# Performance work log

Measured on AMD Instinct MI355X. Metric: run time of the kernel, lower is better.

Reference implementation:

```python
import jax, jax.numpy as jnp
import numpy as np

EPS = 1e-12

def _layernorm(x, gamma, beta):
    m = jnp.mean(x, axis=-1, keepdims=True)
    v = jnp.mean((x - m) ** 2, axis=-1, keepdims=True)
    return (x - m) * jax.lax.rsqrt(v + EPS) * gamma + beta

def _gcn(x, node_emb, time_emb, W_pool, b_pool, gamma, beta):
    # x: [B, N, C]; node_emb: [N, D]; time_emb: [D]
    e = _layernorm(node_emb + time_emb[None, :], gamma, beta)          # [N, D] (dropout off: eval mode)
    A = jax.nn.softmax(e @ e.T, axis=1)                                 # [N, N] dynamic adjacency
    weights = jnp.einsum('nd,dkio->nkio', e, W_pool)                    # [N, 2, C, O] node-adaptive weights
    bias = e @ b_pool                                                   # [N, O]
    # supports = [I, A]; I support is identity -> x itself
    x_g = jnp.stack([x, jnp.einsum('nm,bmc->bnc', A, x)], axis=2)       # [B, N, 2, C]
    return jnp.einsum('bnki,nkio->bno', x_g, weights) + bias            # [B, N, O]

def setup_inputs() -> dict:
    key = jax.random.key(0)
    ks = jax.random.split(key, 16)
    B, N, Din, H, D = 64, 2048, 2, 64, 16
    C = Din + H
    inp = {
        'x': jax.random.normal(ks[0], (B, N, Din), jnp.float32),
        'state': jax.random.normal(ks[1], (B, N, H), jnp.float32),
        'node_embeddings': jax.random.normal(ks[2], (N, D), jnp.float32),
        'time_embeddings': jax.random.normal(ks[3], (D,), jnp.float32),
    }
    for i, g in enumerate(['z', 'r', 'u']):
        inp[f'W_{g}'] = jax.random.normal(ks[4 + 2 * i], (D, 2, C, H), jnp.float32) * 0.02
        inp[f'b_{g}'] = jax.random.normal(ks[5 + 2 * i], (D, H), jnp.float32) * 0.02
        inp[f'gamma_{g}'] = jnp.ones((D,), jnp.float32)
        inp[f'beta_{g}'] = jnp.zeros((D,), jnp.float32)
    return inp

def reference(x, state, node_embeddings, time_embeddings,
              W_z, b_z, gamma_z, beta_z,
              W_r, b_r, gamma_r, beta_r,
              W_u, b_u, gamma_u, beta_u):
    xs = jnp.concatenate([x, state], axis=-1)                           # [B, N, Din+H]
    z = jax.nn.sigmoid(_gcn(xs, node_embeddings, time_embeddings, W_z, b_z, gamma_z, beta_z))
    r = jax.nn.sigmoid(_gcn(xs, node_embeddings, time_embeddings, W_r, b_r, gamma_r, beta_r))
    cand = jnp.concatenate([x, z * state], axis=-1)
    hc = jnp.tanh(_gcn(cand, node_embeddings, time_embeddings, W_u, b_u, gamma_u, beta_u))
    return r * state + (1.0 - r) * hc
```

## Files before the change

### kernel.cpp

```cpp
#include <hip/hip_runtime.h>
#include <hip/hip_bf16.h>
#include <math.h>


typedef __attribute__((ext_vector_type(4))) float f4;
typedef __attribute__((ext_vector_type(8))) short s8;

#define B_   64
#define N_   2048
#define DIN  2
#define H_   64
#define D_   16
#define C_   66
#define KI   132
#define KIP  160
#define CB   4224

#define GLD16(gp, lp) __builtin_amdgcn_global_load_lds((const __attribute__((address_space(1))) void*)(gp), (__attribute__((address_space(3))) void*)(lp), 16, 0, 0)

static __device__ __forceinline__ ushort f2bf(float v) {
  __hip_bfloat16 h = __float2bfloat16(v);
  return *(ushort*)&h;
}
static __device__ __forceinline__ float bf2f(ushort u) {
  __hip_bfloat16 h = *(__hip_bfloat16*)&u;
  return __bfloat162float(h);
}
static __device__ __forceinline__ uint packbf(float a, float b) {
  return ((uint)f2bf(b) << 16) | f2bf(a);
}

__global__ void k_e(const float* __restrict__ node, const float* __restrict__ timee,
                    const float* __restrict__ g0, const float* __restrict__ b0,
                    const float* __restrict__ g1, const float* __restrict__ b1,
                    const float* __restrict__ g2, const float* __restrict__ b2,
                    float* __restrict__ e) {
  int n = blockIdx.x * blockDim.x + threadIdx.x;
  if (n >= N_) return;
  float v[D_]; float m = 0.f;
  #pragma unroll
  for (int d = 0; d < D_; ++d) { v[d] = node[n * D_ + d] + timee[d]; m += v[d]; }
  m *= (1.0f / D_);
  float var = 0.f;
  #pragma unroll
  for (int d = 0; d < D_; ++d) { float t = v[d] - m; var += t * t; }
  var *= (1.0f / D_);
  float r = rsqrtf(var + 1e-12f);
  #pragma unroll
  for (int d = 0; d < D_; ++d) {
    float y = (v[d] - m) * r;
    e[0 * N_ * D_ + n * D_ + d] = y * g0[d] + b0[d];
    e[1 * N_ * D_ + n * D_ + d] = y * g1[d] + b1[d];
    e[2 * N_ * D_ + n * D_ + d] = y * g2[d] + b2[d];
  }
}

__global__ __launch_bounds__(256)
void k_S(const float* __restrict__ e, float* __restrict__ S) {
  __shared__ __align__(16) ushort At[128 * 32];
  __shared__ __align__(16) ushort Bt[128 * 32];
  const int t = threadIdx.x;
  const int c0 = blockIdx.x * 128, r0 = blockIdx.y * 128;
  const float* eg = e + (size_t)blockIdx.z * (N_ * D_);
  float* Sg = S + (size_t)blockIdx.z * ((size_t)N_ * N_);
  const int row = t >> 1, half = t & 1;
  {
    const float* p = eg + (size_t)(r0 + row) * D_ + half * 8;
    float4 a = *(const float4*)p, b = *(const float4*)(p + 4);
    ushort pk[8] = {f2bf(a.x), f2bf(a.y), f2bf(a.z), f2bf(a.w), f2bf(b.x), f2bf(b.y), f2bf(b.z), f2bf(b.w)};
    *(uint4*)&At[row * 32 + half * 8] = *(uint4*)pk;
    uint4 z = {0, 0, 0, 0};
    *(uint4*)&At[row * 32 + 16 + half * 8] = z;
    const float* q2 = eg + (size_t)(c0 + row) * D_ + half * 8;
    float4 c = *(const float4*)q2, d = *(const float4*)(q2 + 4);
    ushort pk2[8] = {f2bf(c.x), f2bf(c.y), f2bf(c.z), f2bf(c.w), f2bf(d.x), f2bf(d.y), f2bf(d.z), f2bf(d.w)};
    *(uint4*)&Bt[row * 32 + half * 8] = *(uint4*)pk2;
    *(uint4*)&Bt[row * 32 + 16 + half * 8] = z;
  }
  __syncthreads();
  const int l15 = t & 15, q = (t >> 4) & 3, w = t >> 6;
  const int wr = (w >> 1) * 64, wc = (w & 1) * 64;
  s8 af[4], bf[4];
  #pragma unroll
  for (int mi = 0; mi < 4; ++mi) af[mi] = *(const s8*)&At[(wr + mi * 16 + l15) * 32 + q * 8];
  #pragma unroll
  for (int ni = 0; ni < 4; ++ni) bf[ni] = *(const s8*)&Bt[(wc + ni * 16 + l15) * 32 + q * 8];
  f4 acc[4][4];
  #pragma unroll
  for (int i = 0; i < 4; ++i)
    #pragma unroll
    for (int j = 0; j < 4; ++j) acc[i][j] = (f4)0.0f;
  #pragma unroll
  for (int mi = 0; mi < 4; ++mi)
    #pragma unroll
    for (int ni = 0; ni < 4; ++ni)
      acc[mi][ni] = __builtin_amdgcn_mfma_f32_16x16x32_bf16(af[mi], bf[ni], acc[mi][ni], 0, 0, 0);
  #pragma unroll
  for (int mi = 0; mi < 4; ++mi) {
    int rr = r0 + wr + mi * 16 + q * 4;
    #pragma unroll
    for (int ni = 0; ni < 4; ++ni) {
      int cc = c0 + wc + ni * 16 + l15;
      #pragma unroll
      for (int rg = 0; rg < 4; ++rg)
        Sg[(size_t)(rr + rg) * N_ + cc] = acc[mi][ni][rg];
    }
  }
}

__global__ __launch_bounds__(256)
void k_rowsm(const float* __restrict__ S, __hip_bfloat16* __restrict__ A) {
  __shared__ float red[256];
  const int r = blockIdx.x, t = threadIdx.x;
  const float* Sr = S + (size_t)blockIdx.z * ((size_t)N_ * N_) + (size_t)r * N_;
  float4 v0 = ((const float4*)Sr)[t];
  float4 v1 = ((const float4*)Sr)[t + 256];
  float mx = fmaxf(fmaxf(fmaxf(v0.x, v0.y), fmaxf(v0.z, v0.w)),
                   fmaxf(fmaxf(v1.x, v1.y), fmaxf(v1.z, v1.w)));
  red[t] = mx; __syncthreads();
  for (int st = 128; st > 0; st >>= 1) { if (t < st) red[t] = fmaxf(red[t], red[t + st]); __syncthreads(); }
  const float gmax = red[0]; __syncthreads();
  float e0 = __expf(v0.x - gmax), e1 = __expf(v0.y - gmax), e2 = __expf(v0.z - gmax), e3 = __expf(v0.w - gmax);
  float e4 = __expf(v1.x - gmax), e5 = __expf(v1.y - gmax), e6 = __expf(v1.z - gmax), e7 = __expf(v1.w - gmax);
  red[t] = e0 + e1 + e2 + e3 + e4 + e5 + e6 + e7; __syncthreads();
  for (int st = 128; st > 0; st >>= 1) { if (t < st) red[t] += red[t + st]; __syncthreads(); }
  const float inv = 1.0f / red[0];
  ushort* Ar = (ushort*)A + (size_t)blockIdx.z * ((size_t)N_ * N_) + (size_t)r * N_;
  ushort p0[4] = {f2bf(e0 * inv), f2bf(e1 * inv), f2bf(e2 * inv), f2bf(e3 * inv)};
  ushort p1[4] = {f2bf(e4 * inv), f2bf(e5 * inv), f2bf(e6 * inv), f2bf(e7 * inv)};
  *(uint2*)&Ar[t * 4] = *(uint2*)p0;
  *(uint2*)&Ar[1024 + t * 4] = *(uint2*)p1;
}

template <int MODE>
__global__ __launch_bounds__(256)
void k_buildX(const float* __restrict__ x, const float* __restrict__ state,
              const __hip_bfloat16* __restrict__ zbuf, __hip_bfloat16* __restrict__ XT) {
  constexpr int LDM = 72;
  __shared__ __align__(16) ushort T[C_ * LDM];
  const int t = threadIdx.x;
  const int m0 = blockIdx.x * 64, b = blockIdx.y;
  const int m = t >> 2, hq = t & 3;
  {
    const float* sp = state + ((size_t)b * N_ + m0 + m) * H_ + hq * 16;
    float sv[16];
    #pragma unroll
    for (int i = 0; i < 16; i += 4) {
      float4 v = *(const float4*)(sp + i);
      sv[i] = v.x; sv[i + 1] = v.y; sv[i + 2] = v.z; sv[i + 3] = v.w;
    }
    if (MODE) {
      const ushort* zp = (const ushort*)zbuf + ((size_t)b * N_ + m0 + m) * H_ + hq * 16;
      uint4 z0 = *(const uint4*)&zp[0], z1 = *(const uint4*)&zp[8];
      uint zw[8] = {z0.x, z0.y, z0.z, z0.w, z1.x, z1.y, z1.z, z1.w};
      #pragma unroll
      for (int i = 0; i < 8; ++i) {
        sv[2 * i]     *= bf2f((ushort)(zw[i] & 0xffffu));
        sv[2 * i + 1] *= bf2f((ushort)(zw[i] >> 16));
      }
    }
    #pragma unroll
    for (int i = 0; i < 16; ++i) T[(DIN + hq * 16 + i) * LDM + m] = f2bf(sv[i]);
    if (t < 64) {
      const float2 xv = *(const float2*)&x[((size_t)b * N_ + m0 + t) * DIN];
      T[0 * LDM + t] = f2bf(xv.x);
      T[1 * LDM + t] = f2bf(xv.y);
    }
  }
  __syncthreads();
  {
    int r = t >> 2, ch = t & 3;
    ushort* dst = (ushort*)XT + (size_t)(b * C_ + r) * N_ + m0 + ch * 16;
    *(uint4*)&dst[0] = *(uint4*)&T[r * LDM + ch * 16];
    *(uint4*)&dst[8] = *(uint4*)&T[r * LDM + ch * 16 + 8];
    if (t < 8) {
      r = 64 + (t >> 2);
      ushort* dst2 = (ushort*)XT + (size_t)(b * C_ + r) * N_ + m0 + ch * 16;
      *(uint4*)&dst2[0] = *(uint4*)&T[r * LDM + ch * 16];
      *(uint4*)&dst2[8] = *(uint4*)&T[r * LDM + ch * 16 + 8];
    }
  }
}

__global__ __launch_bounds__(256)
void k_gemm(const __hip_bfloat16* __restrict__ Abase, size_t astride,
            const __hip_bfloat16* __restrict__ XT,
            __hip_bfloat16* __restrict__ Ybase, size_t ystride) {
  __shared__ __align__(16) ushort At[128 * 32];
  __shared__ __align__(16) ushort Xt[128 * 32];
  const int t = threadIdx.x;
  const int j0 = blockIdx.x * 128, r0 = blockIdx.y * 128;
  const ushort* Ag = (const ushort*)Abase + (size_t)blockIdx.z * astride;
  ushort* Y = (ushort*)Ybase + (size_t)blockIdx.z * ystride;
  const int lane = t & 63, w = t >> 6;
  const int rowa = w * 32 + (lane >> 2), kc = (lane & 3) * 8;
  const ushort* gA = Ag + (size_t)(r0 + rowa) * N_ + kc;
  const ushort* gX = (const ushort*)XT + (size_t)(j0 + rowa) * N_ + kc;
  ushort* lA0 = &At[(w * 32) * 32];
  ushort* lA1 = &At[(w * 32 + 16) * 32];
  ushort* lX0 = &Xt[(w * 32) * 32];
  ushort* lX1 = &Xt[(w * 32 + 16) * 32];
  const int l15 = t & 15, q = (t >> 4) & 3;
  const int wr = (w >> 1) * 64, wc = (w & 1) * 64;
  f4 acc[4][4];
  #pragma unroll
  for (int i = 0; i < 4; ++i)
    #pragma unroll
    for (int jj = 0; jj < 4; ++jj) acc[i][jj] = (f4)0.0f;
  for (int k0 = 0; k0 < N_; k0 += 32) {
    __syncthreads();
    GLD16(gA + k0, lA0);
    GLD16(gA + 16 * N_ + k0, lA1);
    GLD16(gX + k0, lX0);
    GLD16(gX + 16 * N_ + k0, lX1);
    __syncthreads();
    s8 af[4], bf[4];
    #pragma unroll
    for (int mi = 0; mi < 4; ++mi) af[mi] = *(const s8*)&At[(wr + mi * 16 + l15) * 32 + q * 8];
    #pragma unroll
    for (int ni = 0; ni < 4; ++ni) bf[ni] = *(const s8*)&Xt[(wc + ni * 16 + l15) * 32 + q * 8];
    #pragma unroll
    for (int mi = 0; mi < 4; ++mi)
      #pragma unroll
      for (int ni = 0; ni < 4; ++ni)
        acc[mi][ni] = __builtin_amdgcn_mfma_f32_16x16x32_bf16(af[mi], bf[ni], acc[mi][ni], 0, 0, 0);
  }
  #pragma unroll
  for (int mi = 0; mi < 4; ++mi) {
    int rr = r0 + wr + mi * 16 + q * 4;
    #pragma unroll
    for (int ni = 0; ni < 4; ++ni) {
      int cc = j0 + wc + ni * 16 + l15;
      #pragma unroll
      for (int rg = 0; rg < 4; ++rg)
        Y[(size_t)(rr + rg) * CB + cc] = f2bf(acc[mi][ni][rg]);
    }
  }
}

__global__ __launch_bounds__(256)
void k_wmat(const float* __restrict__ eg, const float* __restrict__ Wp, ushort* __restrict__ Wm) {
  constexpr int TRS = 36;
  __shared__ float Wl[16 * 8 * 64];
  __shared__ ushort Tr[8 * 64 * TRS];
  const int t = threadIdx.x;
  const int n0 = blockIdx.x * 8;
  const int y = blockIdx.y;
  const int o = t & 63, w = t >> 6;
  const int ng = w & 1, krh = (w >> 1) * 4;
  float er[4][16];
  #pragma unroll
  for (int j = 0; j < 4; ++j) {
    const float* ep = eg + (size_t)(n0 + ng * 4 + j) * D_;
    #pragma unroll
    for (int d = 0; d < D_; d += 4) {
      float4 v = *(const float4*)(ep + d);
      er[j][d] = v.x; er[j][d + 1] = v.y; er[j][d + 2] = v.z; er[j][d + 3] = v.w;
    }
  }
  const int ngroups = (y == 3) ? 2 : 1;
  for (int g = 0; g < ngroups; ++g) {
    const int kic0 = y * 4 + g * 4;
    for (int kk = 0; kk < 4; ++kk) {
      const int kic = kic0 + kk;
      __syncthreads();
      #pragma unroll
      for (int it = 0; it < 8; ++it) {
        int f = it * 256 + t;
        int d = f >> 7, rem = f & 127, kr = rem >> 4, o4 = rem & 15;
        int ki = kic * 8 + kr;
        float4 v;
        if (ki < KI) v = *(const float4*)&Wp[((size_t)d * KI + ki) * 64 + o4 * 4];
        else { v.x = 0.f; v.y = 0.f; v.z = 0.f; v.w = 0.f; }
        *(float4*)&Wl[f * 4] = v;
      }
      __syncthreads();
      float a[4][4];
      #pragma unroll
      for (int j = 0; j < 4; ++j)
        #pragma unroll
        for (int k = 0; k < 4; ++k) a[j][k] = 0.f;
      for (int d = 0; d < D_; ++d) {
        float w4[4];
        #pragma unroll
        for (int k = 0; k < 4; ++k) w4[k] = Wl[(d * 8 + krh + k) * 64 + o];
        #pragma unroll
        for (int j = 0; j < 4; ++j)
          #pragma unroll
          for (int k = 0; k < 4; ++k) a[j][k] = fmaf(er[j][d], w4[k], a[j][k]);
      }
      #pragma unroll
      for (int j = 0; j < 4; ++j) {
        ushort* tr = &Tr[((ng * 4 + j) * 64 + o) * TRS + kk * 8 + krh];
        *(uint*)&tr[0] = packbf(a[j][0], a[j][1]);
        *(uint*)&tr[2] = packbf(a[j][2], a[j][3]);
      }
    }
    __syncthreads();
    const int k0 = kic0 * 8;
    #pragma unroll
    for (int p = 0; p < 8; ++p) {
      int u = p * 256 + t;
      int nl = u >> 8, oo = (u >> 2) & 63, q = u & 3;
      const ushort* tr = &Tr[(nl * 64 + oo) * TRS + q * 8];
      uint2 lo = *(const uint2*)&tr[0];
      uint2 hi = *(const uint2*)&tr[4];
      uint4 vv; vv.x = lo.x; vv.y = lo.y; vv.z = hi.x; vv.w = hi.y;
      *(uint4*)&Wm[((size_t)(n0 + nl) * 64 + oo) * KIP + k0 + q * 8] = vv;
    }
  }
}

template <int MODE>
__global__ __launch_bounds__(256)
void k_einsum(const float* __restrict__ e, const ushort* __restrict__ Wm, const float* __restrict__ bp,
              const __hip_bfloat16* __restrict__ Y,
              const float* __restrict__ x, const float* __restrict__ state,
              const __hip_bfloat16* __restrict__ zbuf, const __hip_bfloat16* __restrict__ rbuf,
              void* __restrict__ outp) {
  constexpr int LDK = 168;
  constexpr int LDR = 72;
  __shared__ __align__(16) ushort xg[64 * LDK];
  __shared__ __align__(16) ushort res[64 * LDR];
  __shared__ float el[D_];
  __shared__ float bl[64];
  const int n = blockIdx.x, t = threadIdx.x;
  if (t < D_) el[t] = e[n * D_ + t];
  __syncthreads();
  if (t < 64) {
    float s = 0.f;
    #pragma unroll
    for (int d = 0; d < D_; ++d) s += el[d] * bp[d * 64 + t];
    bl[t] = s;
  }
  {
    const int b = t >> 2, j = t & 3;
    const size_t bn = (size_t)b * N_ + n;
    float sv[16];
    const float* sp = state + bn * 64 + j * 16;
    #pragma unroll
    for (int i = 0; i < 16; i += 4) {
      float4 v = *(const float4*)(sp + i);
      sv[i] = v.x; sv[i + 1] = v.y; sv[i + 2] = v.z; sv[i + 3] = v.w;
    }
    if (MODE) {
      const ushort* zp = (const ushort*)zbuf + bn * 64 + j * 16;
      uint4 z0 = *(const uint4*)&zp[0], z1 = *(const uint4*)&zp[8];
      uint zw[8] = {z0.x, z0.y, z0.z, z0.w, z1.x, z1.y, z1.z, z1.w};
      #pragma unroll
      for (int i = 0; i < 8; ++i) {
        sv[2 * i]     *= bf2f((ushort)(zw[i] & 0xffffu));
        sv[2 * i + 1] *= bf2f((ushort)(zw[i] >> 16));
      }
    }
    ushort* xr = &xg[b * LDK + 2 + j * 16];
    #pragma unroll
    for (int i = 0; i < 16; i += 2) {
      uint pk = packbf(sv[i], sv[i + 1]);
      *(uint*)&xr[i] = pk;
    }
    const ushort* yp = (const ushort*)Y + (size_t)n * CB + b * C_ + j * 16;
    uint* xy = (uint*)&xg[b * LDK + 66 + j * 16];
    #pragma unroll
    for (int i = 0; i < 8; ++i) xy[i] = *(const uint*)&yp[2 * i];
    if (j == 0) *(uint*)&xg[b * LDK + 130] = *(const uint*)&yp[64];
    if (t < 64) {
      const float* xp = x + ((size_t)t * N_ + n) * DIN;
      uint pk = packbf(xp[0], xp[1]);
      *(uint*)&xg[t * LDK] = pk;
    }
    ushort* pg = &xg[b * LDK + 132 + j * 7];
    #pragma unroll
    for (int i = 0; i < 7; ++i) pg[i] = 0;
  }
  __syncthreads();
  const int l15 = t & 15, q = (t >> 4) & 3, w = t >> 6;
  const int wm = (w >> 1) * 32, wn = (w & 1) * 32;
  const ushort* Wn = Wm + (size_t)n * (64 * KIP);
  f4 acc[2][2];
  acc[0][0] = acc[0][1] = acc[1][0] = acc[1][1] = (f4)0.0f;
  #pragma unroll
  for (int kk = 0; kk < KIP; kk += 32) {
    s8 af[2], bfr[2];
    #pragma unroll
    for (int mi = 0; mi < 2; ++mi) af[mi] = *(const s8*)&xg[(wm + mi * 16 + l15) * LDK + kk + q * 8];
    #pragma unroll
    for (int ni = 0; ni < 2; ++ni) bfr[ni] = *(const s8*)(Wn + (size_t)(wn + ni * 16 + l15) * KIP + kk + q * 8);
    #pragma unroll
    for (int mi = 0; mi < 2; ++mi)
      #pragma unroll
      for (int ni = 0; ni < 2; ++ni)
        acc[mi][ni] = __builtin_amdgcn_mfma_f32_16x16x32_bf16(af[mi], bfr[ni], acc[mi][ni], 0, 0, 0);
  }
  {
    float bl0 = bl[wn + l15], bl1 = bl[wn + 16 + l15];
    #pragma unroll
    for (int mi = 0; mi < 2; ++mi)
      #pragma unroll
      for (int ni = 0; ni < 2; ++ni) {
        float bb = ni ? bl1 : bl0;
        #pragma unroll
        for (int rg = 0; rg < 4; ++rg) {
          float v = acc[mi][ni][rg] + bb;
          float a;
          if (MODE == 0) a = 1.0f / (1.0f + __expf(-v));
          else           a = 1.0f - 2.0f / (__expf(2.0f * v) + 1.0f);
          res[(wm + mi * 16 + q * 4 + rg) * LDR + (wn + ni * 16 + l15)] = f2bf(a);
        }
      }
  }
  __syncthreads();
  {
    const int b = t >> 2, j = t & 3;
    const size_t gb = ((size_t)b * N_ + n) * 64 + j * 16;
    const ushort* rr = &res[b * LDR + j * 16];
    if (MODE == 0) {
      uint4 v0 = *(const uint4*)&rr[0];
      uint4 v1 = *(const uint4*)&rr[8];
      *(uint4*)((ushort*)outp + gb) = v0;
      *(uint4*)((ushort*)outp + gb + 8) = v1;
    } else {
      float* ob = (float*)outp;
      const float* stp = state + gb;
      const ushort* rp = (const ushort*)rbuf + gb;
      uint4 r0 = *(const uint4*)&rp[0], r1 = *(const uint4*)&rp[8];
      uint rw[8] = {r0.x, r0.y, r0.z, r0.w, r1.x, r1.y, r1.z, r1.w};
      #pragma unroll
      for (int i = 0; i < 16; i += 4) {
        float4 st = *(const float4*)(stp + i);
        float4 ov;
        float rv0 = bf2f((ushort)(rw[i / 2] & 0xffffu));
        float rv1 = bf2f((ushort)(rw[i / 2] >> 16));
        float rv2 = bf2f((ushort)(rw[i / 2 + 1] & 0xffffu));
        float rv3 = bf2f((ushort)(rw[i / 2 + 1] >> 16));
        ov.x = rv0 * st.x + (1.0f - rv0) * bf2f(rr[i]);
        ov.y = rv1 * st.y + (1.0f - rv1) * bf2f(rr[i + 1]);
        ov.z = rv2 * st.z + (1.0f - rv2) * bf2f(rr[i + 2]);
        ov.w = rv3 * st.w + (1.0f - rv3) * bf2f(rr[i + 3]);
        *(float4*)(ob + gb + i) = ov;
      }
    }
  }
}

extern "C" void kernel_launch(void* const* d_in, const int* in_sizes, int n_in,
                              void* d_out, int out_size, void* d_ws, size_t ws_size,
                              hipStream_t stream) {
  const float* x     = (const float*)d_in[0];
  const float* state = (const float*)d_in[1];
  const float* node  = (const float*)d_in[2];
  const float* timee = (const float*)d_in[3];
  const float* W_z = (const float*)d_in[4];
  const float* b_z = (const float*)d_in[5];
  const float* g_z = (const float*)d_in[6];
  const float* be_z = (const float*)d_in[7];
  const float* W_r = (const float*)d_in[8];
  const float* b_r = (const float*)d_in[9];
  const float* g_r = (const float*)d_in[10];
  const float* be_r = (const float*)d_in[11];
  const float* W_u = (const float*)d_in[12];
  const float* b_u = (const float*)d_in[13];
  const float* g_u = (const float*)d_in[14];
  const float* be_u = (const float*)d_in[15];

  constexpr size_t NN = (size_t)N_ * N_;
  constexpr size_t ND = (size_t)N_ * D_;
  char* ws = (char*)d_ws;
  float*           e  = (float*)(ws);
  __hip_bfloat16*  A  = (__hip_bfloat16*)(ws + 393216);
  __hip_bfloat16*  XT = (__hip_bfloat16*)(ws + 25559040);
  __hip_bfloat16*  Y  = (__hip_bfloat16*)(ws + 42860544);
  __hip_bfloat16*  zb = (__hip_bfloat16*)(ws + 60162048);
  __hip_bfloat16*  rb = (__hip_bfloat16*)(ws + 76939264);
  float*           S  = (float*)(ws + 93716480);
  ushort*          Wm = (ushort*)(ws + 93716480);
  __hip_bfloat16*  Yr = (__hip_bfloat16*)(ws + 135659520);
  const size_t YRD = ((size_t)135659520 - 42860544) / 2;
  const bool big = ws_size >= (size_t)152961024;

  float* out = (float*)d_out;

  k_e<<<8, 256, 0, stream>>>(node, timee, g_z, be_z, g_r, be_r, g_u, be_u, e);
  if (big) {
    k_S<<<dim3(16, 16, 3), 256, 0, stream>>>(e, S);
    k_rowsm<<<dim3(N_, 1, 3), 256, 0, stream>>>(S, A);
  } else {
    for (int g = 0; g < 3; ++g) {
      k_S<<<dim3(16, 16, 1), 256, 0, stream>>>(e + g * ND, S);
      k_rowsm<<<dim3(N_, 1, 1), 256, 0, stream>>>(S, A + g * NN);
    }
  }
  k_buildX<0><<<dim3(32, 64), 256, 0, stream>>>(x, state, nullptr, XT);

  dim3 ggrid1(CB / 128, N_ / 128, 1);
  dim3 ggrid2(CB / 128, N_ / 128, 2);
  dim3 wgrid(N_ / 8, 4);

  if (big) {
    k_wmat<<<wgrid, 256, 0, stream>>>(e + 0 * ND, W_z, Wm);
    k_gemm<<<ggrid2, 256, 0, stream>>>(A, NN, XT, Y, YRD);
    k_einsum<0><<<N_, 256, 0, stream>>>(e + 0 * ND, Wm, b_z, Y, x, state, nullptr, nullptr, (void*)zb);
    k_wmat<<<wgrid, 256, 0, stream>>>(e + 1 * ND, W_r, Wm);
    k_einsum<0><<<N_, 256, 0, stream>>>(e + 1 * ND, Wm, b_r, Yr, x, state, nullptr, nullptr, (void*)rb);
  } else {
    k_wmat<<<wgrid, 256, 0, stream>>>(e + 0 * ND, W_z, Wm);
    k_gemm<<<ggrid1, 256, 0, stream>>>(A, 0, XT, Y, 0);
    k_einsum<0><<<N_, 256, 0, stream>>>(e + 0 * ND, Wm, b_z, Y, x, state, nullptr, nullptr, (void*)zb);
    k_wmat<<<wgrid, 256, 0, stream>>>(e + 1 * ND, W_r, Wm);
    k_gemm<<<ggrid1, 256, 0, stream>>>(A + NN, 0, XT, Y, 0);
    k_einsum<0><<<N_, 256, 0, stream>>>(e + 1 * ND, Wm, b_r, Y, x, state, nullptr, nullptr, (void*)rb);
  }
  k_buildX<1><<<dim3(32, 64), 256, 0, stream>>>(x, state, zb, XT);
  k_wmat<<<wgrid, 256, 0, stream>>>(e + 2 * ND, W_u, Wm);
  k_gemm<<<ggrid1, 256, 0, stream>>>(A + 2 * NN, 0, XT, Y, 0);
  k_einsum<1><<<N_, 256, 0, stream>>>(e + 2 * ND, Wm, b_u, Y, x, state, zb, rb, (void*)out);
}
```

Baseline: 490.4 us.

## Fuse score GEMM with row softmax and double-buffer the A×X GEMM

Replaces the separate S=e·eᵀ kernel and row-softmax kernel with one k_attn kernel. It keeps all bf16 embeddings in LDS, computes 16 full rows per block with MFMA and applies the softmax in registers, so the fp32 S matrix is never written to or read from global memory. The k_gemm loop now double-buffers its LDS tiles with async global_load_lds prefetch and remaps workgroups through an XCD-style swizzle. The cost is a 64KB LDS footprint per block, which lowers occupancy, and scattered 2-byte stores of A.

```diff
diff --git a/kernel.cpp b/kernel.cpp
--- a/kernel.cpp
+++ b/kernel.cpp
@@ -34,7 +34,7 @@
                     const float* __restrict__ g0, const float* __restrict__ b0,
                     const float* __restrict__ g1, const float* __restrict__ b1,
                     const float* __restrict__ g2, const float* __restrict__ b2,
-                    float* __restrict__ e) {
+                    float* __restrict__ e, ushort* __restrict__ ebf) {
   int n = blockIdx.x * blockDim.x + threadIdx.x;
   if (n >= N_) return;
   float v[D_]; float m = 0.f;
@@ -46,90 +46,104 @@
   for (int d = 0; d < D_; ++d) { float t = v[d] - m; var += t * t; }
   var *= (1.0f / D_);
   float r = rsqrtf(var + 1e-12f);
-  #pragma unroll
-  for (int d = 0; d < D_; ++d) {
-    float y = (v[d] - m) * r;
-    e[0 * N_ * D_ + n * D_ + d] = y * g0[d] + b0[d];
-    e[1 * N_ * D_ + n * D_ + d] = y * g1[d] + b1[d];
-    e[2 * N_ * D_ + n * D_ + d] = y * g2[d] + b2[d];
+  float y[D_];
+  #pragma unroll
+  for (int d = 0; d < D_; ++d) y[d] = (v[d] - m) * r;
+  const float* gs[3] = {g0, g1, g2};
+  const float* bs[3] = {b0, b1, b2};
+  #pragma unroll
+  for (int g = 0; g < 3; ++g) {
+    #pragma unroll
+    for (int d = 0; d < D_; d += 2) {
+      float o0 = y[d] * gs[g][d] + bs[g][d];
+      float o1 = y[d + 1] * gs[g][d + 1] + bs[g][d + 1];
+      e[g * N_ * D_ + n * D_ + d] = o0;
+      e[g * N_ * D_ + n * D_ + d + 1] = o1;
+      *(uint*)&ebf[g * N_ * D_ + n * D_ + d] = packbf(o0, o1);
+    }
   }
 }
 
 __global__ __launch_bounds__(256)
-void k_S(const float* __restrict__ e, float* __restrict__ S) {
-  __shared__ __align__(16) ushort At[128 * 32];
-  __shared__ __align__(16) ushort Bt[128 * 32];
+void k_attn(const ushort* __restrict__ ebf, __hip_bfloat16* __restrict__ A) {
+  __shared__ __align__(16) ushort eb[N_ * D_];
+  __shared__ float red[4][16];
   const int t = threadIdx.x;
-  const int c0 = blockIdx.x * 128, r0 = blockIdx.y * 128;
-  const float* eg = e + (size_t)blockIdx.z * (N_ * D_);
-  float* Sg = S + (size_t)blockIdx.z * ((size_t)N_ * N_);
-  const int row = t >> 1, half = t & 1;
+  const ushort* eg = ebf + (size_t)blockIdx.z * (N_ * D_);
   {
-    const float* p = eg + (size_t)(r0 + row) * D_ + half * 8;
-    float4 a = *(const float4*)p, b = *(const float4*)(p + 4);
-    ushort pk[8] = {f2bf(a.x), f2bf(a.y), f2bf(a.z), f2bf(a.w), f2bf(b.x), f2bf(b.y), f2bf(b.z), f2bf(b.w)};
-    *(uint4*)&At[row * 32 + half * 8] = *(uint4*)pk;
-    uint4 z = {0, 0, 0, 0};
-    *(uint4*)&At[row * 32 + 16 + half * 8] = z;
-    const float* q2 = eg + (size_t)(c0 + row) * D_ + half * 8;
-    float4 c = *(const float4*)q2, d = *(const float4*)(q2 + 4);
-    ushort pk2[8] = {f2bf(c.x), f2bf(c.y), f2bf(c.z), f2bf(c.w), f2bf(d.x), f2bf(d.y), f2bf(d.z), f2bf(d.w)};
-    *(uint4*)&Bt[row * 32 + half * 8] = *(uint4*)pk2;
-    *(uint4*)&Bt[row * 32 + 16 + half * 8] = z;
-  }
-  __syncthreads();
-  const int l15 = t & 15, q = (t >> 4) & 3, w = t >> 6;
-  const int wr = (w >> 1) * 64, wc = (w & 1) * 64;
-  s8 af[4], bf[4];
-  #pragma unroll
-  for (int mi = 0; mi < 4; ++mi) af[mi] = *(const s8*)&At[(wr + mi * 16 + l15) * 32 + q * 8];
-  #pragma unroll
-  for (int ni = 0; ni < 4; ++ni) bf[ni] = *(const s8*)&Bt[(wc + ni * 16 + l15) * 32 + q * 8];
-  f4 acc[4][4];
-  #pragma unroll
-  for (int i = 0; i < 4; ++i)
-    #pragma unroll
-    for (int j = 0; j < 4; ++j) acc[i][j] = (f4)0.0f;
-  #pragma unroll
-  for (int mi = 0; mi < 4; ++mi)
-    #pragma unroll
-    for (int ni = 0; ni < 4; ++ni)
-      acc[mi][ni] = __builtin_amdgcn_mfma_f32_16x16x32_bf16(af[mi], bf[ni], acc[mi][ni], 0, 0, 0);
-  #pragma unroll
-  for (int mi = 0; mi < 4; ++mi) {
-    int rr = r0 + wr + mi * 16 + q * 4;
-    #pragma unroll
-    for (int ni = 0; ni < 4; ++ni) {
-      int cc = c0 + wc + ni * 16 + l15;
-      #pragma unroll
-      for (int rg = 0; rg < 4; ++rg)
-        Sg[(size_t)(rr + rg) * N_ + cc] = acc[mi][ni][rg];
-    }
-  }
-}
-
-__global__ __launch_bounds__(256)
-void k_rowsm(const float* __restrict__ S, __hip_bfloat16* __restrict__ A) {
-  __shared__ float red[256];
-  const int r = blockIdx.x, t = threadIdx.x;
-  const float* Sr = S + (size_t)blockIdx.z * ((size_t)N_ * N_) + (size_t)r * N_;
-  float4 v0 = ((const float4*)Sr)[t];
-  float4 v1 = ((const float4*)Sr)[t + 256];
-  float mx = fmaxf(fmaxf(fmaxf(v0.x, v0.y), fmaxf(v0.z, v0.w)),
-                   fmaxf(fmaxf(v1.x, v1.y), fmaxf(v1.z, v1.w)));
-  red[t] = mx; __syncthreads();
-  for (int st = 128; st > 0; st >>= 1) { if (t < st) red[t] = fmaxf(red[t], red[t + st]); __syncthreads(); }
-  const float gmax = red[0]; __syncthreads();
-  float e0 = __expf(v0.x - gmax), e1 = __expf(v0.y - gmax), e2 = __expf(v0.z - gmax), e3 = __expf(v0.w - gmax);
-  float e4 = __expf(v1.x - gmax), e5 = __expf(v1.y - gmax), e6 = __expf(v1.z - gmax), e7 = __expf(v1.w - gmax);
-  red[t] = e0 + e1 + e2 + e3 + e4 + e5 + e6 + e7; __syncthreads();
-  for (int st = 128; st > 0; st >>= 1) { if (t < st) red[t] += red[t + st]; __syncthreads(); }
-  const float inv = 1.0f / red[0];
-  ushort* Ar = (ushort*)A + (size_t)blockIdx.z * ((size_t)N_ * N_) + (size_t)r * N_;
-  ushort p0[4] = {f2bf(e0 * inv), f2bf(e1 * inv), f2bf(e2 * inv), f2bf(e3 * inv)};
-  ushort p1[4] = {f2bf(e4 * inv), f2bf(e5 * inv), f2bf(e6 * inv), f2bf(e7 * inv)};
-  *(uint2*)&Ar[t * 4] = *(uint2*)p0;
-  *(uint2*)&Ar[1024 + t * 4] = *(uint2*)p1;
+    const uint4* src = (const uint4*)eg;
+    uint4* dst = (uint4*)eb;
+    #pragma unroll
+    for (int i = 0; i < 16; ++i) dst[i * 256 + t] = src[i * 256 + t];
+  }
+  __syncthreads();
+  const int lane = t & 63, w = t >> 6;
+  const int l15 = lane & 15, q = lane >> 4;
+  const int r0 = blockIdx.x * 16;
+  s8 af = {0, 0, 0, 0, 0, 0, 0, 0};
+  if (q < 2) af = *(const s8*)&eb[(r0 + l15) * D_ + q * 8];
+  const int c0 = w * 512;
+  f4 acc[32];
+  #pragma unroll
+  for (int tl = 0; tl < 32; ++tl) {
+    s8 bfr = {0, 0, 0, 0, 0, 0, 0, 0};
+    if (q < 2) bfr = *(const s8*)&eb[(c0 + tl * 16 + l15) * D_ + q * 8];
+    acc[tl] = __builtin_amdgcn_mfma_f32_16x16x32_bf16(af, bfr, (f4)0.0f, 0, 0, 0);
+  }
+  float pm[4], gm[4];
+  #pragma unroll
+  for (int rg = 0; rg < 4; ++rg) {
+    float m = acc[0][rg];
+    #pragma unroll
+    for (int tl = 1; tl < 32; ++tl) m = fmaxf(m, acc[tl][rg]);
+    m = fmaxf(m, __shfl_xor(m, 1, 64));
+    m = fmaxf(m, __shfl_xor(m, 2, 64));
+    m = fmaxf(m, __shfl_xor(m, 4, 64));
+    m = fmaxf(m, __shfl_xor(m, 8, 64));
+    pm[rg] = m;
+  }
+  if (l15 == 0) {
+    #pragma unroll
+    for (int rg = 0; rg < 4; ++rg) red[w][q * 4 + rg] = pm[rg];
+  }
+  __syncthreads();
+  #pragma unroll
+  for (int rg = 0; rg < 4; ++rg)
+    gm[rg] = fmaxf(fmaxf(red[0][q * 4 + rg], red[1][q * 4 + rg]),
+                   fmaxf(red[2][q * 4 + rg], red[3][q * 4 + rg]));
+  __syncthreads();
+  float ps[4] = {0.f, 0.f, 0.f, 0.f};
+  #pragma unroll
+  for (int tl = 0; tl < 32; ++tl) {
+    #pragma unroll
+    for (int rg = 0; rg < 4; ++rg) {
+      float v = __expf(acc[tl][rg] - gm[rg]);
+      acc[tl][rg] = v;
+      ps[rg] += v;
+    }
+  }
+  #pragma unroll
+  for (int rg = 0; rg < 4; ++rg) {
+    float s = ps[rg];
+    s += __shfl_xor(s, 1, 64);
+    s += __shfl_xor(s, 2, 64);
+    s += __shfl_xor(s, 4, 64);
+    s += __shfl_xor(s, 8, 64);
+    if (l15 == 0) red[w][q * 4 + rg] = s;
+  }
+  __syncthreads();
+  float inv[4];
+  #pragma unroll
+  for (int rg = 0; rg < 4; ++rg)
+    inv[rg] = 1.0f / (red[0][q * 4 + rg] + red[1][q * 4 + rg] +
+                      red[2][q * 4 + rg] + red[3][q * 4 + rg]);
+  ushort* Ar = (ushort*)A + (size_t)blockIdx.z * ((size_t)N_ * N_);
+  #pragma unroll
+  for (int tl = 0; tl < 32; ++tl) {
+    #pragma unroll
+    for (int rg = 0; rg < 4; ++rg)
+      Ar[(size_t)(r0 + q * 4 + rg) * N_ + c0 + tl * 16 + l15] = f2bf(acc[tl][rg] * inv[rg]);
+  }
 }
 
 template <int MODE>
@@ -186,20 +200,24 @@
 void k_gemm(const __hip_bfloat16* __restrict__ Abase, size_t astride,
             const __hip_bfloat16* __restrict__ XT,
             __hip_bfloat16* __restrict__ Ybase, size_t ystride) {
-  __shared__ __align__(16) ushort At[128 * 32];
-  __shared__ __align__(16) ushort Xt[128 * 32];
+  __shared__ __align__(16) ushort At[2][128 * 32];
+  __shared__ __align__(16) ushort Xt[2][128 * 32];
   const int t = threadIdx.x;
-  const int j0 = blockIdx.x * 128, r0 = blockIdx.y * 128;
-  const ushort* Ag = (const ushort*)Abase + (size_t)blockIdx.z * astride;
-  ushort* Y = (ushort*)Ybase + (size_t)blockIdx.z * ystride;
+  const int nwg = gridDim.x * gridDim.y * gridDim.z;
+  const int orig = blockIdx.x + gridDim.x * (blockIdx.y + gridDim.y * blockIdx.z);
+  const int chunk = nwg >> 3;
+  const int swz = (orig & 7) * chunk + (orig >> 3);
+  const int bx = swz % gridDim.x;
+  const int rest = swz / gridDim.x;
+  const int by = rest % gridDim.y;
+  const int bz = rest / gridDim.y;
+  const int j0 = bx * 128, r0 = by * 128;
+  const ushort* Ag = (const ushort*)Abase + (size_t)bz * astride;
+  ushort* Y = (ushort*)Ybase + (size_t)bz * ystride;
   const int lane = t & 63, w = t >> 6;
   const int rowa = w * 32 + (lane >> 2), kc = (lane & 3) * 8;
   const ushort* gA = Ag + (size_t)(r0 + rowa) * N_ + kc;
   const ushort* gX = (const ushort*)XT + (size_t)(j0 + rowa) * N_ + kc;
-  ushort* lA0 = &At[(w * 32) * 32];
-  ushort* lA1 = &At[(w * 32 + 16) * 32];
-  ushort* lX0 = &Xt[(w * 32) * 32];
-  ushort* lX1 = &Xt[(w * 32 + 16) * 32];
   const int l15 = t & 15, q = (t >> 4) & 3;
   const int wr = (w >> 1) * 64, wc = (w & 1) * 64;
   f4 acc[4][4];
@@ -207,23 +225,33 @@
   for (int i = 0; i < 4; ++i)
     #pragma unroll
     for (int jj = 0; jj < 4; ++jj) acc[i][jj] = (f4)0.0f;
+  GLD16(gA, &At[0][(w * 32) * 32]);
+  GLD16(gA + 16 * N_, &At[0][(w * 32 + 16) * 32]);
+  GLD16(gX, &Xt[0][(w * 32) * 32]);
+  GLD16(gX + 16 * N_, &Xt[0][(w * 32 + 16) * 32]);
+  __syncthreads();
+  int cur = 0;
   for (int k0 = 0; k0 < N_; k0 += 32) {
+    const int kn = k0 + 32;
+    if (kn < N_) {
+      const int nx = cur ^ 1;
+      GLD16(gA + kn, &At[nx][(w * 32) * 32]);
+      GLD16(gA + 16 * N_ + kn, &At[nx][(w * 32 + 16) * 32]);
+      GLD16(gX + kn, &Xt[nx][(w * 32) * 32]);
+      GLD16(gX + 16 * N_ + kn, &Xt[nx][(w * 32 + 16) * 32]);
+    }
+    s8 af[4], bfr[4];
+    #pragma unroll
+    for (int mi = 0; mi < 4; ++mi) af[mi] = *(const s8*)&At[cur][(wr + mi * 16 + l15) * 32 + q * 8];
+    #pragma unroll
+    for (int ni = 0; ni < 4; ++ni) bfr[ni] = *(const s8*)&Xt[cur][(wc + ni * 16 + l15) * 32 + q * 8];
+    #pragma unroll
+    for (int mi = 0; mi < 4; ++mi)
+      #pragma unroll
+      for (int ni = 0; ni < 4; ++ni)
+        acc[mi][ni] = __builtin_amdgcn_mfma_f32_16x16x32_bf16(af[mi], bfr[ni], acc[mi][ni], 0, 0, 0);
     __syncthreads();
-    GLD16(gA + k0, lA0);
-    GLD16(gA + 16 * N_ + k0, lA1);
-    GLD16(gX + k0, lX0);
-    GLD16(gX + 16 * N_ + k0, lX1);
-    __syncthreads();
-    s8 af[4], bf[4];
-    #pragma unroll
-    for (int mi = 0; mi < 4; ++mi) af[mi] = *(const s8*)&At[(wr + mi * 16 + l15) * 32 + q * 8];
-    #pragma unroll
-    for (int ni = 0; ni < 4; ++ni) bf[ni] = *(const s8*)&Xt[(wc + ni * 16 + l15) * 32 + q * 8];
-    #pragma unroll
-    for (int mi = 0; mi < 4; ++mi)
-      #pragma unroll
-      for (int ni = 0; ni < 4; ++ni)
-        acc[mi][ni] = __builtin_amdgcn_mfma_f32_16x16x32_bf16(af[mi], bf[ni], acc[mi][ni], 0, 0, 0);
+    cur ^= 1;
   }
   #pragma unroll
   for (int mi = 0; mi < 4; ++mi) {
@@ -301,12 +329,12 @@
     #pragma unroll
     for (int p = 0; p < 8; ++p) {
       int u = p * 256 + t;
-      int nl = u >> 8, oo = (u >> 2) & 63, q = u & 3;
-      const ushort* tr = &Tr[(nl * 64 + oo) * TRS + q * 8];
+      int nl = u >> 8, oo = (u >> 2) & 63, qq = u & 3;
+      const ushort* tr = &Tr[(nl * 64 + oo) * TRS + qq * 8];
       uint2 lo = *(const uint2*)&tr[0];
       uint2 hi = *(const uint2*)&tr[4];
       uint4 vv; vv.x = lo.x; vv.y = lo.y; vv.z = hi.x; vv.w = hi.y;
-      *(uint4*)&Wm[((size_t)(n0 + nl) * 64 + oo) * KIP + k0 + q * 8] = vv;
+      *(uint4*)&Wm[((size_t)(n0 + nl) * 64 + oo) * KIP + k0 + qq * 8] = vv;
     }
   }
 }
@@ -472,7 +500,7 @@
   __hip_bfloat16*  Y  = (__hip_bfloat16*)(ws + 42860544);
   __hip_bfloat16*  zb = (__hip_bfloat16*)(ws + 60162048);
   __hip_bfloat16*  rb = (__hip_bfloat16*)(ws + 76939264);
-  float*           S  = (float*)(ws + 93716480);
+  ushort*          ebf = (ushort*)(ws + 93716480);
   ushort*          Wm = (ushort*)(ws + 93716480);
   __hip_bfloat16*  Yr = (__hip_bfloat16*)(ws + 135659520);
   const size_t YRD = ((size_t)135659520 - 42860544) / 2;
@@ -480,16 +508,8 @@
 
   float* out = (float*)d_out;
 
-  k_e<<<8, 256, 0, stream>>>(node, timee, g_z, be_z, g_r, be_r, g_u, be_u, e);
-  if (big) {
-    k_S<<<dim3(16, 16, 3), 256, 0, stream>>>(e, S);
-    k_rowsm<<<dim3(N_, 1, 3), 256, 0, stream>>>(S, A);
-  } else {
-    for (int g = 0; g < 3; ++g) {
-      k_S<<<dim3(16, 16, 1), 256, 0, stream>>>(e + g * ND, S);
-      k_rowsm<<<dim3(N_, 1, 1), 256, 0, stream>>>(S, A + g * NN);
-    }
-  }
+  k_e<<<8, 256, 0, stream>>>(node, timee, g_z, be_z, g_r, be_r, g_u, be_u, e, ebf);
+  k_attn<<<dim3(N_ / 16, 1, 3), 256, 0, stream>>>(ebf, A);
   k_buildX<0><<<dim3(32, 64), 256, 0, stream>>>(x, state, nullptr, XT);
 
   dim3 ggrid1(CB / 128, N_ / 128, 1);
```

Result: slower. 502.1 us (+2.4%).
